# Optimization experiments

Measured on AMD Instinct MI355X. Metric: run time of the kernel, lower is better.

## Reference

```python
import jax, jax.numpy as jnp
import numpy as np

D_MODEL = 4096
NUM_EXPERTS = 64
TOP_K = 2


def setup_inputs() -> dict:
    key = jax.random.key(0)
    kx, kw, kb = jax.random.split(key, 3)
    x = jax.random.normal(kx, (4, 4096, D_MODEL), dtype=jnp.float32)
    # nn.Linear(d_model, num_experts): weight [E, D], bias [E]
    bound = 1.0 / np.sqrt(D_MODEL)
    W = jax.random.uniform(kw, (NUM_EXPERTS, D_MODEL), jnp.float32, -bound, bound)
    b = jax.random.uniform(kb, (NUM_EXPERTS,), jnp.float32, -bound, bound)
    return {"x": x, "W": W, "b": b}


def reference(x, W, b):
    # gate: logits over experts  [B, S, E]
    logits = jnp.einsum("bsd,ed->bse", x, W) + b
    # top-k experts per token
    top_w, top_i = jax.lax.top_k(logits, TOP_K)  # [B, S, K]
    # softmax over the selected k logits
    top_w = jax.nn.softmax(top_w, axis=-1)
    return top_w, top_i
```

## Files before the change

kernel.cpp:

```cpp
#include <hip/hip_runtime.h>
#include <math.h>

#define D_MODEL 4096
#define NE 64
#define TPB 64
#define NSTEPS 64
#define BUFB 32768
#define NBUF 5
#define WS_SHORTS (256 * 2 * 64 * 8)

typedef __attribute__((ext_vector_type(8))) short short8;
typedef __attribute__((ext_vector_type(16))) float f32x16;

__device__ __forceinline__ void gl_lds(const void* g, void* l) {
    __builtin_amdgcn_global_load_lds(
        (const __attribute__((address_space(1))) unsigned*)g,
        (__attribute__((address_space(3))) unsigned*)l, 16, 0, 0);
}

__device__ __forceinline__ void split8(const float4& a, const float4& c,
                                       short8& h8, short8& l8) {
    union { short8 s; unsigned u[4]; } H, L;
    float vv[8] = {a.x, a.y, a.z, a.w, c.x, c.y, c.z, c.w};
#pragma unroll
    for (int p = 0; p < 4; p++) {
        const float v0 = vv[2*p], v1 = vv[2*p+1];
        const unsigned u0 = __float_as_uint(v0), u1 = __float_as_uint(v1);
        const unsigned r0 = u0 + 0x7fffu + ((u0 >> 16) & 1u);
        const unsigned r1 = u1 + 0x7fffu + ((u1 >> 16) & 1u);
        const float lo0 = v0 - __uint_as_float(r0 & 0xffff0000u);
        const float lo1 = v1 - __uint_as_float(r1 & 0xffff0000u);
        H.u[p] = __builtin_amdgcn_perm(r1, r0, 0x07060302u);
        L.u[p] = __builtin_amdgcn_perm(__float_as_uint(lo1),
                                       __float_as_uint(lo0), 0x07060302u);
    }
    h8 = H.s; l8 = L.s;
}

__global__ void wsplit_kernel(const float* __restrict__ W, short* __restrict__ wsp) {
    const int ck = blockIdx.x, t = threadIdx.x;
    const int nt = t >> 6, l = t & 63;
    const float* wp = W + (size_t)(nt * 32 + (l & 31)) * D_MODEL + ck * 16 + (l >> 5) * 8;
    float4 a = *(const float4*)wp, c = *(const float4*)(wp + 4);
    union { short8 s; unsigned u[4]; } H, L;
    float vv[8] = {a.x, a.y, a.z, a.w, c.x, c.y, c.z, c.w};
#pragma unroll
    for (int p = 0; p < 4; p++) {
        const float v0 = vv[2*p], v1 = vv[2*p+1];
        const unsigned u0 = __float_as_uint(v0), u1 = __float_as_uint(v1);
        const unsigned r0 = u0 + 0x7fffu + ((u0 >> 16) & 1u);
        const unsigned r1 = u1 + 0x7fffu + ((u1 >> 16) & 1u);
        const float lo0 = v0 - __uint_as_float(r0 & 0xffff0000u);
        const float lo1 = v1 - __uint_as_float(r1 & 0xffff0000u);
        const unsigned q0 = __float_as_uint(lo0) + 0x7fffu + ((__float_as_uint(lo0) >> 16) & 1u);
        const unsigned q1 = __float_as_uint(lo1) + 0x7fffu + ((__float_as_uint(lo1) >> 16) & 1u);
        H.u[p] = __builtin_amdgcn_perm(r1, r0, 0x07060302u);
        L.u[p] = __builtin_amdgcn_perm(q1, q0, 0x07060302u);
    }
    const size_t off = ((size_t)(ck * 2 + nt) * 64 + l) * 8;
    *(short8*)(wsp + off)             = H.s;
    *(short8*)(wsp + WS_SHORTS + off) = L.s;
}

#define MF(A_, B_, n_) acc[n_] = __builtin_amdgcn_mfma_f32_32x32x16_bf16( \
                             A_, B_, acc[n_], 0, 0, 0)

__global__ __launch_bounds__(512) void router_pipe(
    const float* __restrict__ x, const short* __restrict__ wsp,
    const float* __restrict__ b, float* __restrict__ out, int T)
{
    __shared__ char smem[NBUF * BUFB];

    const int tid  = threadIdx.x;
    const int wv   = tid >> 6, lane = tid & 63;
    const int mt   = wv & 1;
    const int kq   = wv >> 1;
    const int tok0 = blockIdx.x * TPB;

    const int tokA = tid >> 4, clA = tid & 15;
    const int tokB = 32 + tokA;
    const float* gx1 = x + (size_t)(tok0 + tokA) * D_MODEL + ((clA ^ (tokA & 15)) * 4);
    const float* gx2 = x + (size_t)(tok0 + tokB) * D_MODEL + ((clA ^ (tokB & 15)) * 4);
    const char* whi = (const char*)wsp + (size_t)tid * 16;
    const char* wlo = (const char*)(wsp + WS_SHORTS) + (size_t)tid * 16;

    auto stage = [&](int sc, int bi) {
        char* db = smem + bi * BUFB + wv * 1024;
        gl_lds(gx1 + (size_t)sc * 64, db);
        gl_lds(gx2 + (size_t)sc * 64, db + 8192);
        gl_lds(whi + (size_t)sc * 8192, db + 16384);
        gl_lds(wlo + (size_t)sc * 8192, db + 24576);
    };

    f32x16 acc[2];
#pragma unroll
    for (int e = 0; e < 16; e++) { acc[0][e] = 0.f; acc[1][e] = 0.f; }

    const int row = mt * 32 + (lane & 31);
    const int c0  = kq * 4 + (lane >> 5) * 2;
    const int xo1 = row * 256 + ((c0     ^ (row & 15)) * 16);
    const int xo2 = row * 256 + (((c0+1) ^ (row & 15)) * 16);
    const int wo0 = 16384 + ((kq * 2 + 0) * 64 + lane) * 16;
    const int wo1 = 16384 + ((kq * 2 + 1) * 64 + lane) * 16;

    auto compute = [&](int bi) {
        const char* buf = smem + bi * BUFB;
        float4 xa = *(const float4*)(buf + xo1);
        float4 xb = *(const float4*)(buf + xo2);
        short8 b0h = *(const short8*)(buf + wo0);
        short8 b1h = *(const short8*)(buf + wo1);
        short8 b0l = *(const short8*)(buf + wo0 + 8192);
        short8 b1l = *(const short8*)(buf + wo1 + 8192);
        short8 Ah, Al;
        split8(xa, xb, Ah, Al);
        MF(Ah, b0h, 0); MF(Ah, b0l, 0); MF(Al, b0h, 0); MF(Al, b0l, 0);
        MF(Ah, b1h, 1); MF(Ah, b1l, 1); MF(Al, b1h, 1); MF(Al, b1l, 1);
    };

    stage(0, 0); stage(1, 1); stage(2, 2);

    int bs = 3, bc = 0;
    for (int s = 0; s < NSTEPS - 3; ++s) {
        stage(s + 3, bs);
        asm volatile("s_waitcnt vmcnt(12)" ::: "memory");
        __builtin_amdgcn_s_barrier();
        __builtin_amdgcn_sched_barrier(0);
        compute(bc);
        if (++bs == NBUF) bs = 0;
        if (++bc == NBUF) bc = 0;
    }
    asm volatile("s_waitcnt vmcnt(8)" ::: "memory");
    __builtin_amdgcn_s_barrier();
    __builtin_amdgcn_sched_barrier(0);
    compute(bc); if (++bc == NBUF) bc = 0;
    asm volatile("s_waitcnt vmcnt(4)" ::: "memory");
    __builtin_amdgcn_s_barrier();
    __builtin_amdgcn_sched_barrier(0);
    compute(bc); if (++bc == NBUF) bc = 0;
    asm volatile("s_waitcnt vmcnt(0)" ::: "memory");
    __builtin_amdgcn_s_barrier();
    __builtin_amdgcn_sched_barrier(0);
    compute(bc);

    __syncthreads();

    float* red = (float*)smem;
    auto store_slab = [&](int slab) {
        float* sl = red + ((size_t)slab * 64 + lane) * 32;
#pragma unroll
        for (int q = 0; q < 8; q++) {
            const int nt = q >> 2, rg = (q & 3) * 4;
            *(float4*)(sl + ((q + lane) & 7) * 4) =
                make_float4(acc[nt][rg], acc[nt][rg+1], acc[nt][rg+2], acc[nt][rg+3]);
        }
    };
    auto add_slab = [&](int slab) {
        const float* sl = red + ((size_t)slab * 64 + lane) * 32;
#pragma unroll
        for (int q = 0; q < 8; q++) {
            const int nt = q >> 2, rg = (q & 3) * 4;
            float4 v = *(const float4*)(sl + ((q + lane) & 7) * 4);
            acc[nt][rg] += v.x; acc[nt][rg+1] += v.y;
            acc[nt][rg+2] += v.z; acc[nt][rg+3] += v.w;
        }
    };
    if (kq >= 2) store_slab(mt * 2 + (kq - 2));
    __syncthreads();
    if (kq < 2) add_slab(mt * 2 + kq);
    __syncthreads();
    if (kq == 1) store_slab(mt);
    __syncthreads();
    if (kq == 0) add_slab(mt);
    __syncthreads();

    float* lg = (float*)(smem + 49152);
    if (kq == 0) {
        const int h = lane >> 5, c31 = lane & 31;
        const float bb0 = b[c31], bb1 = b[32 + c31];
#pragma unroll
        for (int nt = 0; nt < 2; nt++) {
#pragma unroll
            for (int e = 0; e < 16; e++) {
                const int r2 = (e & 3) + 8 * (e >> 2) + 4 * h;
                lg[(mt * 32 + r2) * 68 + nt * 32 + c31] = acc[nt][e] + (nt ? bb1 : bb0);
            }
        }
    }
    __syncthreads();

    if (tid < TPB) {
        const float4* rowp = (const float4*)(lg + tid * 68);
        float v0 = -INFINITY, v1 = -INFINITY;
        int i0 = 0, i1 = 0;
#pragma unroll
        for (int q = 0; q < 16; q++) {
            float4 v4 = rowp[q];
            float vs[4] = {v4.x, v4.y, v4.z, v4.w};
#pragma unroll
            for (int j = 0; j < 4; j++) {
                const int e = q * 4 + j;
                const float v = vs[j];
                if (v > v0)      { v1 = v0; i1 = i0; v0 = v; i0 = e; }
                else if (v > v1) { v1 = v;  i1 = e; }
            }
        }
        const float e1 = expf(v1 - v0);
        const float w0 = 1.f / (1.f + e1);
        const int tok = tok0 + tid;
        out[tok * 2 + 0] = w0;
        out[tok * 2 + 1] = e1 * w0;
        float* oi = out + (size_t)T * 2;
        oi[tok * 2 + 0] = (float)i0;
        oi[tok * 2 + 1] = (float)i1;
    }
}

__global__ __launch_bounds__(512, 4) void router_fb(
    const float* __restrict__ x, const float* __restrict__ W,
    const float* __restrict__ b, float* __restrict__ out, int T)
{
    __shared__ short smem[16384];
    const int tid = threadIdx.x;
    const int wv = tid >> 6, lane = tid & 63;
    const int tok0 = blockIdx.x * 32;
    const int row = lane & 31, kh = lane >> 5;
    const float* gx = x + (size_t)(tok0 + row) * D_MODEL + wv * 512 + kh * 8;
    f32x16 acc[2];
#pragma unroll
    for (int e = 0; e < 16; e++) { acc[0][e] = 0.f; acc[1][e] = 0.f; }
    for (int s = 0; s < 32; s++) {
        const float* g = gx + (size_t)s * 16;
        float4 xa = *(const float4*)g, xb = *(const float4*)(g + 4);
        const int k0 = wv * 512 + s * 16 + kh * 8;
        const float* w0 = W + (size_t)row * D_MODEL + k0;
        const float* w1 = W + (size_t)(32 + row) * D_MODEL + k0;
        short8 Ah, Al, B0h, B0l, B1h, B1l;
        split8(xa, xb, Ah, Al);
        split8(*(const float4*)w0, *(const float4*)(w0 + 4), B0h, B0l);
        split8(*(const float4*)w1, *(const float4*)(w1 + 4), B1h, B1l);
        MF(Ah, B0h, 0); MF(Ah, B0l, 0); MF(Al, B0h, 0); MF(Al, B0l, 0);
        MF(Ah, B1h, 1); MF(Ah, B1l, 1); MF(Al, B1h, 1); MF(Al, B1l, 1);
    }
    float* red = (float*)smem;
    auto store_slab = [&](int slab) {
        float* sl = red + ((size_t)slab * 64 + lane) * 32;
#pragma unroll
        for (int q = 0; q < 8; q++) {
            const int nt = q >> 2, rg = (q & 3) * 4;
            *(float4*)(sl + ((q + lane) & 7) * 4) =
                make_float4(acc[nt][rg], acc[nt][rg+1], acc[nt][rg+2], acc[nt][rg+3]);
        }
    };
    auto add_slab = [&](int slab) {
        const float* sl = red + ((size_t)slab * 64 + lane) * 32;
#pragma unroll
        for (int q = 0; q < 8; q++) {
            const int nt = q >> 2, rg = (q & 3) * 4;
            float4 v = *(const float4*)(sl + ((q + lane) & 7) * 4);
            acc[nt][rg] += v.x; acc[nt][rg+1] += v.y;
            acc[nt][rg+2] += v.z; acc[nt][rg+3] += v.w;
        }
    };
    __syncthreads();
    if (wv >= 4) store_slab(wv - 4);
    __syncthreads();
    if (wv < 4) add_slab(wv);
    __syncthreads();
    if (wv == 2 || wv == 3) store_slab(wv - 2);
    __syncthreads();
    if (wv < 2) add_slab(wv);
    __syncthreads();
    if (wv == 1) store_slab(0);
    __syncthreads();
    if (wv == 0) add_slab(0);
    __syncthreads();
    float* lg = (float*)smem;
    if (wv == 0) {
        const int h = lane >> 5, c31 = lane & 31;
        const float bb0 = b[c31], bb1 = b[32 + c31];
#pragma unroll
        for (int nt = 0; nt < 2; nt++)
#pragma unroll
            for (int e = 0; e < 16; e++) {
                const int r2 = (e & 3) + 8 * (e >> 2) + 4 * h;
                lg[r2 * 68 + nt * 32 + c31] = acc[nt][e] + (nt ? bb1 : bb0);
            }
    }
    __syncthreads();
    if (tid < 32) {
        const float4* rowp = (const float4*)(lg + tid * 68);
        float v0 = -INFINITY, v1 = -INFINITY;
        int i0 = 0, i1 = 0;
#pragma unroll
        for (int q = 0; q < 16; q++) {
            float4 v4 = rowp[q];
            float vs[4] = {v4.x, v4.y, v4.z, v4.w};
#pragma unroll
            for (int j = 0; j < 4; j++) {
                const float v = vs[j];
                if (v > v0)      { v1 = v0; i1 = i0; v0 = v; i0 = q*4+j; }
                else if (v > v1) { v1 = v;  i1 = q*4+j; }
            }
        }
        const float e1 = expf(v1 - v0);
        const float w0 = 1.f / (1.f + e1);
        const int tok = tok0 + tid;
        out[tok * 2 + 0] = w0;
        out[tok * 2 + 1] = e1 * w0;
        float* oi = out + (size_t)T * 2;
        oi[tok * 2 + 0] = (float)i0;
        oi[tok * 2 + 1] = (float)i1;
    }
}

extern "C" void kernel_launch(void* const* d_in, const int* in_sizes, int n_in,
                              void* d_out, int out_size, void* d_ws, size_t ws_size,
                              hipStream_t stream) {
    const float* x = (const float*)d_in[0];
    const float* W = (const float*)d_in[1];
    const float* b = (const float*)d_in[2];
    float* out = (float*)d_out;
    short* wsp = (short*)d_ws;
    const int T = in_sizes[0] / D_MODEL;

    const bool pre = (ws_size >= (size_t)(2 * WS_SHORTS) * sizeof(short));
    if (pre) {
        hipLaunchKernelGGL(wsplit_kernel, dim3(256), dim3(128), 0, stream, W, wsp);
        hipLaunchKernelGGL(router_pipe, dim3(T / TPB), dim3(512), 0, stream,
                           x, wsp, b, out, T);
    } else {
        hipLaunchKernelGGL(router_fb, dim3(T / 32), dim3(512), 0, stream,
                           x, W, b, out, T);
    }
}
```

Measured before the change: 67.84 us.

## Halve tokens per block, shrink LDS pipeline to raise occupancy

Each block now handles 32 tokens instead of 64. Each wave computes one 32x32 expert tile with a single accumulator, and the LDS ring is cut to three 24KB buffers so more blocks fit per CU (launch bounds now request 4). The pipeline issues its stage after the barrier with a shallower wait, and the cross-wave reduction becomes one store/add pass. In exchange, each block reloads the full weight stream for half as many tokens, which doubles weight traffic, and the prefetch depth is smaller.

```diff
diff --git a/kernel.cpp b/kernel.cpp
--- a/kernel.cpp
+++ b/kernel.cpp
@@ -3,10 +3,10 @@
 
 #define D_MODEL 4096
 #define NE 64
-#define TPB 64
+#define TPB 32
 #define NSTEPS 64
-#define BUFB 32768
-#define NBUF 5
+#define BUFB 24576
+#define NBUF 3
 #define WS_SHORTS (256 * 2 * 64 * 8)
 
 typedef __attribute__((ext_vector_type(8))) short short8;
@@ -62,10 +62,9 @@
     *(short8*)(wsp + WS_SHORTS + off) = L.s;
 }
 
-#define MF(A_, B_, n_) acc[n_] = __builtin_amdgcn_mfma_f32_32x32x16_bf16( \
-                             A_, B_, acc[n_], 0, 0, 0)
-
-__global__ __launch_bounds__(512) void router_pipe(
+#define MF(A_, B_) acc = __builtin_amdgcn_mfma_f32_32x32x16_bf16(A_, B_, acc, 0, 0, 0)
+
+__global__ __launch_bounds__(512, 4) void router_pipe(
     const float* __restrict__ x, const short* __restrict__ wsp,
     const float* __restrict__ b, float* __restrict__ out, int T)
 {
@@ -73,70 +72,57 @@
 
     const int tid  = threadIdx.x;
     const int wv   = tid >> 6, lane = tid & 63;
-    const int mt   = wv & 1;
+    const int nt   = wv & 1;
     const int kq   = wv >> 1;
     const int tok0 = blockIdx.x * TPB;
 
-    const int tokA = tid >> 4, clA = tid & 15;
-    const int tokB = 32 + tokA;
-    const float* gx1 = x + (size_t)(tok0 + tokA) * D_MODEL + ((clA ^ (tokA & 15)) * 4);
-    const float* gx2 = x + (size_t)(tok0 + tokB) * D_MODEL + ((clA ^ (tokB & 15)) * 4);
+    const int stok = tid >> 4, sq = tid & 15;
+    const float* gx = x + (size_t)(tok0 + stok) * D_MODEL + ((sq ^ (stok & 15)) * 4);
     const char* whi = (const char*)wsp + (size_t)tid * 16;
     const char* wlo = (const char*)(wsp + WS_SHORTS) + (size_t)tid * 16;
 
     auto stage = [&](int sc, int bi) {
         char* db = smem + bi * BUFB + wv * 1024;
-        gl_lds(gx1 + (size_t)sc * 64, db);
-        gl_lds(gx2 + (size_t)sc * 64, db + 8192);
-        gl_lds(whi + (size_t)sc * 8192, db + 16384);
-        gl_lds(wlo + (size_t)sc * 8192, db + 24576);
-    };
-
-    f32x16 acc[2];
-#pragma unroll
-    for (int e = 0; e < 16; e++) { acc[0][e] = 0.f; acc[1][e] = 0.f; }
-
-    const int row = mt * 32 + (lane & 31);
+        gl_lds(gx + (size_t)sc * 64, db);
+        gl_lds(whi + (size_t)sc * 8192, db + 8192);
+        gl_lds(wlo + (size_t)sc * 8192, db + 16384);
+    };
+
+    f32x16 acc;
+#pragma unroll
+    for (int e = 0; e < 16; e++) acc[e] = 0.f;
+
+    const int row = lane & 31;
     const int c0  = kq * 4 + (lane >> 5) * 2;
-    const int xo1 = row * 256 + ((c0     ^ (row & 15)) * 16);
-    const int xo2 = row * 256 + (((c0+1) ^ (row & 15)) * 16);
-    const int wo0 = 16384 + ((kq * 2 + 0) * 64 + lane) * 16;
-    const int wo1 = 16384 + ((kq * 2 + 1) * 64 + lane) * 16;
+    const int xo1 = row * 256 + ((c0       ^ (row & 15)) * 16);
+    const int xo2 = row * 256 + (((c0 + 1) ^ (row & 15)) * 16);
+    const int wo  = 8192 + (kq * 2 + nt) * 1024 + lane * 16;
 
     auto compute = [&](int bi) {
         const char* buf = smem + bi * BUFB;
         float4 xa = *(const float4*)(buf + xo1);
         float4 xb = *(const float4*)(buf + xo2);
-        short8 b0h = *(const short8*)(buf + wo0);
-        short8 b1h = *(const short8*)(buf + wo1);
-        short8 b0l = *(const short8*)(buf + wo0 + 8192);
-        short8 b1l = *(const short8*)(buf + wo1 + 8192);
+        short8 Bh = *(const short8*)(buf + wo);
+        short8 Bl = *(const short8*)(buf + wo + 8192);
         short8 Ah, Al;
         split8(xa, xb, Ah, Al);
-        MF(Ah, b0h, 0); MF(Ah, b0l, 0); MF(Al, b0h, 0); MF(Al, b0l, 0);
-        MF(Ah, b1h, 1); MF(Ah, b1l, 1); MF(Al, b1h, 1); MF(Al, b1l, 1);
-    };
-
-    stage(0, 0); stage(1, 1); stage(2, 2);
-
-    int bs = 3, bc = 0;
-    for (int s = 0; s < NSTEPS - 3; ++s) {
-        stage(s + 3, bs);
-        asm volatile("s_waitcnt vmcnt(12)" ::: "memory");
+        MF(Ah, Bh); MF(Ah, Bl); MF(Al, Bh); MF(Al, Bl);
+    };
+
+    stage(0, 0); stage(1, 1);
+
+    int bs = 2, bc = 0;
+    for (int s = 0; s < NSTEPS - 1; ++s) {
+        asm volatile("s_waitcnt vmcnt(3)" ::: "memory");
         __builtin_amdgcn_s_barrier();
         __builtin_amdgcn_sched_barrier(0);
+        if (s + 2 < NSTEPS) {
+            stage(s + 2, bs);
+            if (++bs == NBUF) bs = 0;
+        }
         compute(bc);
-        if (++bs == NBUF) bs = 0;
         if (++bc == NBUF) bc = 0;
     }
-    asm volatile("s_waitcnt vmcnt(8)" ::: "memory");
-    __builtin_amdgcn_s_barrier();
-    __builtin_amdgcn_sched_barrier(0);
-    compute(bc); if (++bc == NBUF) bc = 0;
-    asm volatile("s_waitcnt vmcnt(4)" ::: "memory");
-    __builtin_amdgcn_s_barrier();
-    __builtin_amdgcn_sched_barrier(0);
-    compute(bc); if (++bc == NBUF) bc = 0;
     asm volatile("s_waitcnt vmcnt(0)" ::: "memory");
     __builtin_amdgcn_s_barrier();
     __builtin_amdgcn_sched_barrier(0);
@@ -146,44 +132,34 @@
 
     float* red = (float*)smem;
     auto store_slab = [&](int slab) {
-        float* sl = red + ((size_t)slab * 64 + lane) * 32;
-#pragma unroll
-        for (int q = 0; q < 8; q++) {
-            const int nt = q >> 2, rg = (q & 3) * 4;
-            *(float4*)(sl + ((q + lane) & 7) * 4) =
-                make_float4(acc[nt][rg], acc[nt][rg+1], acc[nt][rg+2], acc[nt][rg+3]);
-        }
+        float* sl = red + ((size_t)slab * 64 + lane) * 16;
+#pragma unroll
+        for (int q = 0; q < 4; q++)
+            *(float4*)(sl + ((q + lane) & 3) * 4) =
+                make_float4(acc[4*q], acc[4*q+1], acc[4*q+2], acc[4*q+3]);
     };
     auto add_slab = [&](int slab) {
-        const float* sl = red + ((size_t)slab * 64 + lane) * 32;
-#pragma unroll
-        for (int q = 0; q < 8; q++) {
-            const int nt = q >> 2, rg = (q & 3) * 4;
-            float4 v = *(const float4*)(sl + ((q + lane) & 7) * 4);
-            acc[nt][rg] += v.x; acc[nt][rg+1] += v.y;
-            acc[nt][rg+2] += v.z; acc[nt][rg+3] += v.w;
-        }
-    };
-    if (kq >= 2) store_slab(mt * 2 + (kq - 2));
-    __syncthreads();
-    if (kq < 2) add_slab(mt * 2 + kq);
-    __syncthreads();
-    if (kq == 1) store_slab(mt);
-    __syncthreads();
-    if (kq == 0) add_slab(mt);
-    __syncthreads();
-
-    float* lg = (float*)(smem + 49152);
+        const float* sl = red + ((size_t)slab * 64 + lane) * 16;
+#pragma unroll
+        for (int q = 0; q < 4; q++) {
+            float4 v = *(const float4*)(sl + ((q + lane) & 3) * 4);
+            acc[4*q] += v.x; acc[4*q+1] += v.y; acc[4*q+2] += v.z; acc[4*q+3] += v.w;
+        }
+    };
+    if (kq > 0) store_slab(nt * 3 + (kq - 1));
+    __syncthreads();
+
+    float* lg = (float*)(smem + 24576);
     if (kq == 0) {
-        const int h = lane >> 5, c31 = lane & 31;
-        const float bb0 = b[c31], bb1 = b[32 + c31];
-#pragma unroll
-        for (int nt = 0; nt < 2; nt++) {
-#pragma unroll
-            for (int e = 0; e < 16; e++) {
-                const int r2 = (e & 3) + 8 * (e >> 2) + 4 * h;
-                lg[(mt * 32 + r2) * 68 + nt * 32 + c31] = acc[nt][e] + (nt ? bb1 : bb0);
-            }
+        add_slab(nt * 3 + 0);
+        add_slab(nt * 3 + 1);
+        add_slab(nt * 3 + 2);
+        const int c31 = lane & 31, h = lane >> 5;
+        const float bb = b[nt * 32 + c31];
+#pragma unroll
+        for (int e = 0; e < 16; e++) {
+            const int r2 = (e & 3) + 8 * (e >> 2) + 4 * h;
+            lg[r2 * 68 + nt * 32 + c31] = acc[e] + bb;
         }
     }
     __syncthreads();
@@ -214,6 +190,10 @@
         oi[tok * 2 + 1] = (float)i1;
     }
 }
+
+#undef MF
+#define MF(A_, B_, n_) acc[n_] = __builtin_amdgcn_mfma_f32_32x32x16_bf16( \
+                             A_, B_, acc[n_], 0, 0, 0)
 
 __global__ __launch_bounds__(512, 4) void router_fb(
     const float* __restrict__ x, const float* __restrict__ W,
```

Result: slower. 84.48 us (+24.5%).
